# Performance work log

Measured on AMD Instinct MI355X. Metric: run time of the kernel, lower is better.

The kernel has to match this reference:

```python
import jax, jax.numpy as jnp
import numpy as np

B, S, D, H = 4, 2048, 1024, 16
HS = D // H  # head_size = 64


def setup_inputs() -> dict:
    key = jax.random.key(0)
    ks = jax.random.split(key, 6)
    scale = 0.02
    return {
        "token_embeddings": jax.random.normal(ks[0], (B, S, D), dtype=jnp.float32),
        # per-head projection weights, stacked: [H, D, HS] (x @ W per head)
        "Wq": jax.random.normal(ks[1], (H, D, HS), dtype=jnp.float32) * scale,
        "Wk": jax.random.normal(ks[2], (H, D, HS), dtype=jnp.float32) * scale,
        "Wv": jax.random.normal(ks[3], (H, D, HS), dtype=jnp.float32) * scale,
        # output projection (Linear with bias): y = x @ Wo + bo
        "Wo": jax.random.normal(ks[4], (D, D), dtype=jnp.float32) * scale,
        "bo": jax.random.normal(ks[5], (D,), dtype=jnp.float32) * scale,
    }


def reference(token_embeddings, Wq, Wk, Wv, Wo, bo):
    # Per-head projections, batched over heads: [B,H,S,HS]
    q = jnp.einsum("bsd,hde->bhse", token_embeddings, Wq)
    k = jnp.einsum("bsd,hde->bhse", token_embeddings, Wk)
    v = jnp.einsum("bsd,hde->bhse", token_embeddings, Wv)
    scale = HS ** -0.5
    scores = jnp.einsum("bhqe,bhke->bhqk", q, k) * scale  # [B,H,S,S]
    causal = jnp.tril(jnp.ones((S, S), dtype=bool))
    scores = jnp.where(causal, scores, -jnp.inf)
    weights = jax.nn.softmax(scores, axis=-1)
    # dropout in eval mode -> identity
    out = jnp.einsum("bhqk,bhke->bhqe", weights, v)  # [B,H,S,HS]
    # concat heads -> [B,S,D] (head order matches torch.cat over heads)
    out = out.transpose(0, 2, 1, 3).reshape(B, S, D)
    return out @ Wo + bo
```

## Files before the change

kernel.cpp:

```cpp
#include <hip/hip_runtime.h>


typedef __bf16 bf16;
typedef bf16 bf16x8 __attribute__((ext_vector_type(8)));
typedef bf16 bf16x4 __attribute__((ext_vector_type(4)));
typedef float f32x4 __attribute__((ext_vector_type(4)));

__device__ __forceinline__ void gload16(const void* gsrc, void* ldst) {
  __builtin_amdgcn_global_load_lds(
      (const __attribute__((address_space(1))) unsigned int*)gsrc,
      (__attribute__((address_space(3))) unsigned int*)ldst, 16, 0, 0);
}

__device__ __forceinline__ f32x4 mfma16(bf16x8 a, bf16x8 b, f32x4 c) {
  return __builtin_amdgcn_mfma_f32_16x16x32_bf16(a, b, c, 0, 0, 0);
}

__global__ __launch_bounds__(256) void pack_all_kernel(const float* __restrict__ x,
                                                       const float* __restrict__ Wq,
                                                       const float* __restrict__ Wk,
                                                       const float* __restrict__ Wv,
                                                       const float* __restrict__ Wo,
                                                       bf16* __restrict__ xb,
                                                       bf16* __restrict__ WT,
                                                       bf16* __restrict__ WoT) {
  const int stride = gridDim.x * 256;
  const int t0 = blockIdx.x * 256 + threadIdx.x;
  for (int i = t0; i < 2097152; i += stride) {
    float4 v = *(const float4*)(x + (size_t)i * 4);
    bf16x4 o;
    o[0] = (bf16)v.x; o[1] = (bf16)v.y; o[2] = (bf16)v.z; o[3] = (bf16)v.w;
    *(bf16x4*)(xb + (size_t)i * 4) = o;
  }
  for (int idx = t0; idx < 3145728; idx += stride) {
    int n = idx >> 10, k = idx & 1023;
    int sel = n >> 10, nn = n & 1023;
    const float* W = (sel == 0) ? Wq : (sel == 1 ? Wk : Wv);
    int h = nn >> 6, e = nn & 63;
    WT[(size_t)n * 1024 + k] = (bf16)W[h * 65536 + k * 64 + e];
  }
  for (int idx = t0; idx < 1048576; idx += stride) {
    int n = idx >> 10, k = idx & 1023;
    WoT[idx] = (bf16)Wo[k * 1024 + n];
  }
}

template <bool F32OUT>
__global__ __launch_bounds__(256, 2) void gemm4_kernel(const bf16* __restrict__ A,
                                                       const bf16* __restrict__ BT,
                                                       bf16* __restrict__ Cb,
                                                       float* __restrict__ Cf,
                                                       const float* __restrict__ bias,
                                                       int N, int K) {
  __shared__ bf16 As[2][128 * 64];
  __shared__ bf16 Bs[2][128 * 64];
  const int tid = threadIdx.x, lane = tid & 63, wave = tid >> 6;
  const int g = lane >> 4, c = lane & 15;
  const int wr = wave >> 1, wc = wave & 1;
  const int bid = blockIdx.x;
  const int xcd = bid & 7, local = bid >> 3;
  const int m0 = (xcd * 8 + (local & 7)) * 128;
  const int n0 = (local >> 3) * 128;

  const int schunk = (lane & 7) ^ (lane >> 3);

#define STAGE4(T, S)                                                      \
  do {                                                                    \
    _Pragma("unroll") for (int j = 0; j < 4; ++j) {                       \
      const int r = wave * 32 + j * 8 + (lane >> 3);                      \
      const int ldso = wave * 4096 + j * 1024 + lane * 16;                \
      gload16(A + (size_t)(m0 + r) * K + (T)*64 + schunk * 8,             \
              (char*)&As[S][0] + ldso);                                   \
      gload16(BT + (size_t)(n0 + r) * K + (T)*64 + schunk * 8,            \
              (char*)&Bs[S][0] + ldso);                                   \
    }                                                                     \
  } while (0)

  f32x4 acc[4][4] = {};
  const int nt = K >> 6;
  STAGE4(0, 0);
  asm volatile("s_waitcnt vmcnt(0)" ::: "memory");
  __builtin_amdgcn_sched_barrier(0);
  __builtin_amdgcn_s_barrier();
  __builtin_amdgcn_sched_barrier(0);

#pragma unroll 1
  for (int t = 0; t < nt; ++t) {
    const int s = t & 1;
    if (t + 1 < nt) STAGE4(t + 1, s ^ 1);
    bf16x8 af[4][2], bfr[4][2];
#pragma unroll
    for (int m = 0; m < 4; ++m) {
      const int row = wr * 64 + m * 16 + c;
#pragma unroll
      for (int kk = 0; kk < 2; ++kk)
        af[m][kk] = *(const bf16x8*)((const char*)&As[s][0] + row * 128 +
                                     (((kk * 4 + g) ^ (row & 7)) << 4));
    }
#pragma unroll
    for (int n = 0; n < 4; ++n) {
      const int row = wc * 64 + n * 16 + c;
#pragma unroll
      for (int kk = 0; kk < 2; ++kk)
        bfr[n][kk] = *(const bf16x8*)((const char*)&Bs[s][0] + row * 128 +
                                      (((kk * 4 + g) ^ (row & 7)) << 4));
    }
    __builtin_amdgcn_s_setprio(1);
#pragma unroll
    for (int kk = 0; kk < 2; ++kk)
#pragma unroll
      for (int m = 0; m < 4; ++m)
#pragma unroll
        for (int n = 0; n < 4; ++n)
          acc[m][n] = mfma16(af[m][kk], bfr[n][kk], acc[m][n]);
    __builtin_amdgcn_s_setprio(0);
    if (t + 1 < nt) {
      asm volatile("s_waitcnt vmcnt(0)" ::: "memory");
      __builtin_amdgcn_sched_barrier(0);
      __builtin_amdgcn_s_barrier();
      __builtin_amdgcn_sched_barrier(0);
    }
  }
#undef STAGE4
#pragma unroll
  for (int m = 0; m < 4; ++m)
#pragma unroll
    for (int n = 0; n < 4; ++n)
#pragma unroll
      for (int i = 0; i < 4; ++i) {
        int row = m0 + wr * 64 + m * 16 + g * 4 + i;
        int col = n0 + wc * 64 + n * 16 + c;
        if (F32OUT)
          Cf[(size_t)row * N + col] = acc[m][n][i] + bias[col];
        else
          Cb[(size_t)row * N + col] = (bf16)acc[m][n][i];
      }
}

__global__ __launch_bounds__(256) void transpose_v_kernel(const bf16* __restrict__ qkv,
                                                          bf16* __restrict__ vt) {
  __shared__ bf16 tl[64][72];
  const int tid = threadIdx.x;
  const int st = blockIdx.x, bh = blockIdx.y;
  const int b = bh >> 4, h = bh & 15;
#pragma unroll
  for (int it = 0; it < 2; ++it) {
    int idx = it * 256 + tid;
    int sl = idx >> 3, ch = idx & 7;
    bf16x8 v = *(const bf16x8*)(qkv + (size_t)(b * 2048 + st * 64 + sl) * 3072 + 2048 + h * 64 + ch * 8);
    *(bf16x8*)&tl[sl][ch * 8] = v;
  }
  __syncthreads();
#pragma unroll
  for (int it = 0; it < 2; ++it) {
    int idx = it * 256 + tid;
    int d = idx >> 3, ch = idx & 7;
    const int blk = ch >> 2, g = ch & 3;
    bf16x8 o;
#pragma unroll
    for (int j = 0; j < 8; ++j) {
      int loc = (j < 4) ? (4 * g + j) : (16 + 4 * g + (j - 4));
      o[j] = tl[blk * 32 + loc][d];
    }
    *(bf16x8*)(vt + ((size_t)bh * 64 + d) * 2048 + st * 64 + ch * 8) = o;
  }
}

__global__ __launch_bounds__(512, 4) void attn_kernel(const bf16* __restrict__ qkv,
                                                      const bf16* __restrict__ vt,
                                                      bf16* __restrict__ attn_out) {
  __shared__ bf16 Ks[2][128 * 64];
  __shared__ bf16 Vs[2][64 * 128];
  const int tid = threadIdx.x, lane = tid & 63, wave = tid >> 6;
  const int g = lane >> 4, c = lane & 15;
  const int bid = blockIdx.x;
  const int xcd = bid & 7;
  const int x = (bid >> 3) & 7;
  const int bh = (bid >> 6) * 8 + xcd;
  const int b = bh >> 4, h = bh & 15;
  const float SCL = 0.125f * 1.4426950408889634f;

  bf16x8 ones;
#pragma unroll
  for (int j = 0; j < 8; ++j) ones[j] = (bf16)1.0f;

#define STAGE(KT, BUF)                                                                    \
  do {                                                                                    \
    _Pragma("unroll") for (int t2 = 0; t2 < 2; ++t2) {                                    \
      int o = t2 * 8192 + wave * 1024 + lane * 16;                          \
      int rK = o >> 7, chK = (((o & 127) >> 4) ^ (rK & 7));                               \
      gload16((const char*)qkv +                                                          \
                  ((size_t)(b * 2048 + (KT)*128 + rK) * 3072 + 1024 + h * 64) * 2 +       \
                  (chK << 4),                                                             \
              (char*)Ks[BUF] + o);                                                        \
      int rV = o >> 8, chV = (((o & 255) >> 4) ^ (rV & 7));                               \
      gload16((const char*)vt + (((size_t)bh * 64 + rV) * 2048 + (KT)*128) * 2 +          \
                  (chV << 4),                                                             \
              (char*)Vs[BUF] + o);                                                        \
    }                                                                                     \
  } while (0)

#pragma unroll 1
  for (int ph = 0; ph < 2; ++ph) {
    const int qt = ph ? (15 - x) : x;
    const int qlow = qt * 128 + wave * 16;

    bf16x8 qf[2];
#pragma unroll
    for (int kk = 0; kk < 2; ++kk) {
      size_t row = (size_t)(b * 2048 + qlow + c);
      qf[kk] = *(const bf16x8*)(qkv + row * 3072 + h * 64 + kk * 32 + g * 8);
    }

    f32x4 oacc[4] = {};
    f32x4 lacc = {};
    float mrun = -3.0e38f;

    const int nkt = qt + 1;
    __builtin_amdgcn_s_barrier();
    __builtin_amdgcn_sched_barrier(0);
    STAGE(0, 0);
    asm volatile("s_waitcnt vmcnt(0)" ::: "memory");
    __builtin_amdgcn_sched_barrier(0);
    __builtin_amdgcn_s_barrier();
    __builtin_amdgcn_sched_barrier(0);
    for (int kt = 0; kt < nkt; ++kt) {
      const int cur = kt & 1;
      if (kt + 1 < nkt) STAGE(kt + 1, cur ^ 1);
      f32x4 sc[8] = {};
      __builtin_amdgcn_s_setprio(1);
#pragma unroll
      for (int n = 0; n < 8; ++n) {
        int key = n * 16 + c;
#pragma unroll
        for (int kk = 0; kk < 2; ++kk) {
          bf16x8 kf = *(const bf16x8*)((const char*)Ks[cur] + key * 128 +
                                       (((kk * 4 + g) ^ (key & 7)) << 4));
          sc[n] = mfma16(kf, qf[kk], sc[n]);
        }
      }
      __builtin_amdgcn_s_setprio(0);
      const int q = qlow + c;
      if (kt == qt) {
#pragma unroll
        for (int n = 0; n < 8; ++n)
#pragma unroll
          for (int i = 0; i < 4; ++i)
            sc[n][i] = ((kt * 128 + n * 16 + 4 * g + i) <= q) ? sc[n][i] : -3.0e38f;
      }
      float vmax;
      {
        float a[8];
#pragma unroll
        for (int n = 0; n < 8; ++n)
          a[n] = fmaxf(fmaxf(sc[n][0], sc[n][1]), fmaxf(sc[n][2], sc[n][3]));
        float b0 = fmaxf(a[0], a[1]), b1 = fmaxf(a[2], a[3]);
        float b2 = fmaxf(a[4], a[5]), b3 = fmaxf(a[6], a[7]);
        vmax = fmaxf(fmaxf(b0, b1), fmaxf(b2, b3));
      }
      vmax = fmaxf(vmax, __shfl_xor(vmax, 16));
      vmax = fmaxf(vmax, __shfl_xor(vmax, 32));
      const float mx = vmax * SCL;
      if (!__all(mx <= mrun + 8.0f)) {
        const float mnew = fmaxf(mrun, mx);
        const float fs = __builtin_amdgcn_exp2f(mrun - mnew);
        mrun = mnew;
#pragma unroll
        for (int i = 0; i < 4; ++i) {
          float fsb = __shfl(fs, ((lane >> 4) << 2) + i);
          lacc[i] *= fsb;
#pragma unroll
          for (int dn = 0; dn < 4; ++dn) oacc[dn][i] *= fsb;
        }
      }
#pragma unroll
      for (int n = 0; n < 8; ++n)
#pragma unroll
        for (int i = 0; i < 4; ++i)
          sc[n][i] = __builtin_amdgcn_exp2f(fmaf(sc[n][i], SCL, -mrun));
      bf16x8 pa[4];
#pragma unroll
      for (int kss = 0; kss < 4; ++kss) {
        bf16x8 t;
#pragma unroll
        for (int j = 0; j < 4; ++j) t[j] = (bf16)sc[2 * kss][j];
#pragma unroll
        for (int j = 0; j < 4; ++j) t[4 + j] = (bf16)sc[2 * kss + 1][j];
        pa[kss] = t;
      }
      __builtin_amdgcn_s_setprio(1);
#pragma unroll
      for (int kss = 0; kss < 4; ++kss) {
        lacc = mfma16(pa[kss], ones, lacc);
#pragma unroll
        for (int dn = 0; dn < 4; ++dn) {
          const int d = dn * 16 + c;
          bf16x8 vb = *(const bf16x8*)((const char*)Vs[cur] + d * 256 +
                                       (((kss * 4 + g) ^ (d & 7)) << 4));
          oacc[dn] = mfma16(pa[kss], vb, oacc[dn]);
        }
      }
      __builtin_amdgcn_s_setprio(0);
      if (kt + 1 < nkt) {
        asm volatile("s_waitcnt vmcnt(0)" ::: "memory");
        __builtin_amdgcn_sched_barrier(0);
        __builtin_amdgcn_s_barrier();
        __builtin_amdgcn_sched_barrier(0);
      }
    }
#pragma unroll
    for (int i = 0; i < 4; ++i) {
      float inv = __builtin_amdgcn_rcpf(lacc[i]);
      size_t row = (size_t)(b * 2048 + qlow + 4 * g + i);
#pragma unroll
      for (int dn = 0; dn < 4; ++dn)
        attn_out[row * 1024 + h * 64 + dn * 16 + c] = (bf16)(oacc[dn][i] * inv);
    }
  }
#undef STAGE
}

extern "C" void kernel_launch(void* const* d_in, const int* in_sizes, int n_in,
                              void* d_out, int out_size, void* d_ws, size_t ws_size,
                              hipStream_t stream) {
  const float* x  = (const float*)d_in[0];
  const float* Wq = (const float*)d_in[1];
  const float* Wk = (const float*)d_in[2];
  const float* Wv = (const float*)d_in[3];
  const float* Wo = (const float*)d_in[4];
  const float* bo = (const float*)d_in[5];
  float* out = (float*)d_out;
  char* ws = (char*)d_ws;

  bf16* Xb    = (bf16*)(ws);
  bf16* WqkvT = (bf16*)(ws + 16777216);
  bf16* WoT   = (bf16*)(ws + 23068672);
  bf16* QKV   = (bf16*)(ws + 25165824);
  bf16* VT    = (bf16*)(ws + 75497472);
  bf16* AttnO = (bf16*)(ws + 92274688);

  pack_all_kernel<<<2048, 256, 0, stream>>>(x, Wq, Wk, Wv, Wo, Xb, WqkvT, WoT);
  gemm4_kernel<false><<<1536, 256, 0, stream>>>(Xb, WqkvT, QKV, nullptr, nullptr,
                                                3072, 1024);
  transpose_v_kernel<<<dim3(32, 64), 256, 0, stream>>>(QKV, VT);
  attn_kernel<<<512, 512, 0, stream>>>(QKV, VT, AttnO);
  gemm4_kernel<true><<<512, 256, 0, stream>>>(AttnO, WoT, nullptr, out, bo,
                                              1024, 1024);
}
```

Baseline: 167.5 us.

## Give each attention wave two query sub-tiles to reuse K/V fragments

```diff
diff --git a/kernel.cpp b/kernel.cpp
--- a/kernel.cpp
+++ b/kernel.cpp
@@ -166,7 +166,7 @@
   }
 }
 
-__global__ __launch_bounds__(512, 4) void attn_kernel(const bf16* __restrict__ qkv,
+__global__ __launch_bounds__(256, 2) void attn_kernel(const bf16* __restrict__ qkv,
                                                       const bf16* __restrict__ vt,
                                                       bf16* __restrict__ attn_out) {
   __shared__ bf16 Ks[2][128 * 64];
@@ -186,8 +186,8 @@
 
 #define STAGE(KT, BUF)                                                                    \
   do {                                                                                    \
-    _Pragma("unroll") for (int t2 = 0; t2 < 2; ++t2) {                                    \
-      int o = t2 * 8192 + wave * 1024 + lane * 16;                          \
+    _Pragma("unroll") for (int t2 = 0; t2 < 4; ++t2) {                                    \
+      int o = t2 * 4096 + wave * 1024 + lane * 16;                          \
       int rK = o >> 7, chK = (((o & 127) >> 4) ^ (rK & 7));                               \
       gload16((const char*)qkv +                                                          \
                   ((size_t)(b * 2048 + (KT)*128 + rK) * 3072 + 1024 + h * 64) * 2 +       \
@@ -203,18 +203,20 @@
 #pragma unroll 1
   for (int ph = 0; ph < 2; ++ph) {
     const int qt = ph ? (15 - x) : x;
-    const int qlow = qt * 128 + wave * 16;
-
-    bf16x8 qf[2];
-#pragma unroll
-    for (int kk = 0; kk < 2; ++kk) {
-      size_t row = (size_t)(b * 2048 + qlow + c);
-      qf[kk] = *(const bf16x8*)(qkv + row * 3072 + h * 64 + kk * 32 + g * 8);
-    }
-
-    f32x4 oacc[4] = {};
-    f32x4 lacc = {};
-    float mrun = -3.0e38f;
+    const int qlow = qt * 128 + wave * 32;
+
+    bf16x8 qf[2][2];
+#pragma unroll
+    for (int m = 0; m < 2; ++m)
+#pragma unroll
+      for (int kk = 0; kk < 2; ++kk) {
+        size_t row = (size_t)(b * 2048 + qlow + m * 16 + c);
+        qf[m][kk] = *(const bf16x8*)(qkv + row * 3072 + h * 64 + kk * 32 + g * 8);
+      }
+
+    f32x4 oacc[2][4] = {};
+    f32x4 lacc[2] = {};
+    float mrun[2] = {-3.0e38f, -3.0e38f};
 
     const int nkt = qt + 1;
     __builtin_amdgcn_s_barrier();
@@ -227,7 +229,7 @@
     for (int kt = 0; kt < nkt; ++kt) {
       const int cur = kt & 1;
       if (kt + 1 < nkt) STAGE(kt + 1, cur ^ 1);
-      f32x4 sc[8] = {};
+      f32x4 sc[8][2] = {};
       __builtin_amdgcn_s_setprio(1);
 #pragma unroll
       for (int n = 0; n < 8; ++n) {
@@ -236,68 +238,79 @@
         for (int kk = 0; kk < 2; ++kk) {
           bf16x8 kf = *(const bf16x8*)((const char*)Ks[cur] + key * 128 +
                                        (((kk * 4 + g) ^ (key & 7)) << 4));
-          sc[n] = mfma16(kf, qf[kk], sc[n]);
+#pragma unroll
+          for (int m = 0; m < 2; ++m) sc[n][m] = mfma16(kf, qf[m][kk], sc[n][m]);
         }
       }
       __builtin_amdgcn_s_setprio(0);
-      const int q = qlow + c;
-      if (kt == qt) {
+      float mx[2];
+#pragma unroll
+      for (int m = 0; m < 2; ++m) {
+        const int q = qlow + m * 16 + c;
+        if (kt == qt) {
+#pragma unroll
+          for (int n = 0; n < 8; ++n)
+#pragma unroll
+            for (int i = 0; i < 4; ++i)
+              sc[n][m][i] = ((kt * 128 + n * 16 + 4 * g + i) <= q) ? sc[n][m][i] : -3.0e38f;
+        }
+        float a[8];
 #pragma unroll
         for (int n = 0; n < 8; ++n)
-#pragma unroll
-          for (int i = 0; i < 4; ++i)
-            sc[n][i] = ((kt * 128 + n * 16 + 4 * g + i) <= q) ? sc[n][i] : -3.0e38f;
-      }
-      float vmax;
-      {
-        float a[8];
-#pragma unroll
-        for (int n = 0; n < 8; ++n)
-          a[n] = fmaxf(fmaxf(sc[n][0], sc[n][1]), fmaxf(sc[n][2], sc[n][3]));
+          a[n] = fmaxf(fmaxf(sc[n][m][0], sc[n][m][1]), fmaxf(sc[n][m][2], sc[n][m][3]));
         float b0 = fmaxf(a[0], a[1]), b1 = fmaxf(a[2], a[3]);
         float b2 = fmaxf(a[4], a[5]), b3 = fmaxf(a[6], a[7]);
-        vmax = fmaxf(fmaxf(b0, b1), fmaxf(b2, b3));
-      }
-      vmax = fmaxf(vmax, __shfl_xor(vmax, 16));
-      vmax = fmaxf(vmax, __shfl_xor(vmax, 32));
-      const float mx = vmax * SCL;
-      if (!__all(mx <= mrun + 8.0f)) {
-        const float mnew = fmaxf(mrun, mx);
-        const float fs = __builtin_amdgcn_exp2f(mrun - mnew);
-        mrun = mnew;
-#pragma unroll
-        for (int i = 0; i < 4; ++i) {
-          float fsb = __shfl(fs, ((lane >> 4) << 2) + i);
-          lacc[i] *= fsb;
-#pragma unroll
-          for (int dn = 0; dn < 4; ++dn) oacc[dn][i] *= fsb;
-        }
-      }
-#pragma unroll
-      for (int n = 0; n < 8; ++n)
-#pragma unroll
-        for (int i = 0; i < 4; ++i)
-          sc[n][i] = __builtin_amdgcn_exp2f(fmaf(sc[n][i], SCL, -mrun));
-      bf16x8 pa[4];
+        float vmax = fmaxf(fmaxf(b0, b1), fmaxf(b2, b3));
+        vmax = fmaxf(vmax, __shfl_xor(vmax, 16));
+        vmax = fmaxf(vmax, __shfl_xor(vmax, 32));
+        mx[m] = vmax * SCL;
+      }
+      if (!__all(mx[0] <= mrun[0] + 8.0f && mx[1] <= mrun[1] + 8.0f)) {
+#pragma unroll
+        for (int m = 0; m < 2; ++m) {
+          const float mnew = fmaxf(mrun[m], mx[m]);
+          const float fs = __builtin_amdgcn_exp2f(mrun[m] - mnew);
+          mrun[m] = mnew;
+#pragma unroll
+          for (int i = 0; i < 4; ++i) {
+            float fsb = __shfl(fs, ((lane >> 4) << 2) + i);
+            lacc[m][i] *= fsb;
+#pragma unroll
+            for (int dn = 0; dn < 4; ++dn) oacc[m][dn][i] *= fsb;
+          }
+        }
+      }
+#pragma unroll
+      for (int m = 0; m < 2; ++m)
+#pragma unroll
+        for (int n = 0; n < 8; ++n)
+#pragma unroll
+          for (int i = 0; i < 4; ++i)
+            sc[n][m][i] = __builtin_amdgcn_exp2f(fmaf(sc[n][m][i], SCL, -mrun[m]));
+      bf16x8 pa[2][4];
+#pragma unroll
+      for (int m = 0; m < 2; ++m)
+#pragma unroll
+        for (int kss = 0; kss < 4; ++kss) {
+          bf16x8 t;
+#pragma unroll
+          for (int j = 0; j < 4; ++j) t[j] = (bf16)sc[2 * kss][m][j];
+#pragma unroll
+          for (int j = 0; j < 4; ++j) t[4 + j] = (bf16)sc[2 * kss + 1][m][j];
+          pa[m][kss] = t;
+        }
+      __builtin_amdgcn_s_setprio(1);
 #pragma unroll
       for (int kss = 0; kss < 4; ++kss) {
-        bf16x8 t;
-#pragma unroll
-        for (int j = 0; j < 4; ++j) t[j] = (bf16)sc[2 * kss][j];
-#pragma unroll
-        for (int j = 0; j < 4; ++j) t[4 + j] = (bf16)sc[2 * kss + 1][j];
-        pa[kss] = t;
-      }
-      __builtin_amdgcn_s_setprio(1);
-#pragma unroll
-      for (int kss = 0; kss < 4; ++kss) {
-        lacc = mfma16(pa[kss], ones, lacc);
+#pragma unroll
+        for (int m = 0; m < 2; ++m) lacc[m] = mfma16(pa[m][kss], ones, lacc[m]);
 #pragma unroll
         for (int dn = 0; dn < 4; ++dn) {
           const int d = dn * 16 + c;
           bf16x8 vb = *(const bf16x8*)((const char*)Vs[cur] + d * 256 +
                                        (((kss * 4 + g) ^ (d & 7)) << 4));
-          oacc[dn] = mfma16(pa[kss], vb, oacc[dn]);
+#pragma unroll
+          for (int m = 0; m < 2; ++m) oacc[m][dn] = mfma16(pa[m][kss], vb, oacc[m][dn]);
         }
       }
       __builtin_amdgcn_s_setprio(0);
@@ -309,13 +322,15 @@
       }
     }
 #pragma unroll
-    for (int i = 0; i < 4; ++i) {
-      float inv = __builtin_amdgcn_rcpf(lacc[i]);
-      size_t row = (size_t)(b * 2048 + qlow + 4 * g + i);
-#pragma unroll
-      for (int dn = 0; dn < 4; ++dn)
-        attn_out[row * 1024 + h * 64 + dn * 16 + c] = (bf16)(oacc[dn][i] * inv);
-    }
+    for (int m = 0; m < 2; ++m)
+#pragma unroll
+      for (int i = 0; i < 4; ++i) {
+        float inv = __builtin_amdgcn_rcpf(lacc[m][i]);
+        size_t row = (size_t)(b * 2048 + qlow + m * 16 + 4 * g + i);
+#pragma unroll
+        for (int dn = 0; dn < 4; ++dn)
+          attn_out[row * 1024 + h * 64 + dn * 16 + c] = (bf16)(oacc[m][dn][i] * inv);
+      }
   }
 #undef STAGE
 }
@@ -343,7 +358,7 @@
   gemm4_kernel<false><<<1536, 256, 0, stream>>>(Xb, WqkvT, QKV, nullptr, nullptr,
                                                 3072, 1024);
   transpose_v_kernel<<<dim3(32, 64), 256, 0, stream>>>(QKV, VT);
-  attn_kernel<<<512, 512, 0, stream>>>(QKV, VT, AttnO);
+  attn_kernel<<<512, 256, 0, stream>>>(QKV, VT, AttnO);
   gemm4_kernel<true><<<512, 256, 0, stream>>>(AttnO, WoT, nullptr, out, bo,
                                               1024, 1024);
 }
```

Measured after the change: 170.0 us. About the same (+1.5%).

## Use 256x256-tile 8-wave GEMM kernel for the QKV projection

Applied to the files above, without the earlier changes.

```diff
diff --git a/kernel.cpp b/kernel.cpp
--- a/kernel.cpp
+++ b/kernel.cpp
@@ -43,6 +43,95 @@
     int n = idx >> 10, k = idx & 1023;
     WoT[idx] = (bf16)Wo[k * 1024 + n];
   }
+}
+
+template <bool F32OUT>
+__global__ __launch_bounds__(512, 2) void gemm7_kernel(const bf16* __restrict__ A,
+                                                       const bf16* __restrict__ BT,
+                                                       bf16* __restrict__ Cb,
+                                                       float* __restrict__ Cf,
+                                                       const float* __restrict__ bias,
+                                                       int N, int K) {
+  __shared__ bf16 As[2][256 * 64];
+  __shared__ bf16 Bs[2][256 * 64];
+  const int tid = threadIdx.x, lane = tid & 63, wave = tid >> 6;
+  const int g = lane >> 4, c = lane & 15;
+  const int wr = wave >> 2, wc = wave & 3;
+  const int bid = blockIdx.x;
+  const int xcd = bid & 7, local = bid >> 3;
+  const int m0 = (xcd * 4 + (local & 3)) * 256;
+  const int n0 = (local >> 2) * 256;
+
+  const int sch = (tid & 7) ^ ((tid >> 3) & 7);
+
+#define STAGE7(T, S)                                                      \
+  do {                                                                    \
+    _Pragma("unroll") for (int j = 0; j < 4; ++j) {                       \
+      const int r = j * 64 + (tid >> 3);                                  \
+      const int ldso = j * 8192 + tid * 16;                               \
+      gload16(A + (size_t)(m0 + r) * K + (T)*64 + sch * 8,                \
+              (char*)&As[S][0] + ldso);                                   \
+      gload16(BT + (size_t)(n0 + r) * K + (T)*64 + sch * 8,               \
+              (char*)&Bs[S][0] + ldso);                                   \
+    }                                                                     \
+  } while (0)
+
+  f32x4 acc[8][4] = {};
+  const int nt = K >> 6;
+  STAGE7(0, 0);
+  asm volatile("s_waitcnt vmcnt(0)" ::: "memory");
+  __builtin_amdgcn_sched_barrier(0);
+  __builtin_amdgcn_s_barrier();
+  __builtin_amdgcn_sched_barrier(0);
+
+#pragma unroll 1
+  for (int t = 0; t < nt; ++t) {
+    const int s = t & 1;
+    if (t + 1 < nt) STAGE7(t + 1, s ^ 1);
+#pragma unroll
+    for (int kk = 0; kk < 2; ++kk) {
+      bf16x8 af[8], bfr[4];
+#pragma unroll
+      for (int m = 0; m < 8; ++m) {
+        const int row = wr * 128 + m * 16 + c;
+        af[m] = *(const bf16x8*)((const char*)&As[s][0] + row * 128 +
+                                 (((kk * 4 + g) ^ (row & 7)) << 4));
+      }
+#pragma unroll
+      for (int n = 0; n < 4; ++n) {
+        const int row = wc * 64 + n * 16 + c;
+        bfr[n] = *(const bf16x8*)((const char*)&Bs[s][0] + row * 128 +
+                                  (((kk * 4 + g) ^ (row & 7)) << 4));
+      }
+      __builtin_amdgcn_s_setprio(1);
+#pragma unroll
+      for (int m = 0; m < 8; ++m)
+#pragma unroll
+        for (int n = 0; n < 4; ++n)
+          acc[m][n] = mfma16(af[m], bfr[n], acc[m][n]);
+      __builtin_amdgcn_s_setprio(0);
+    }
+    if (t + 1 < nt) {
+      asm volatile("s_waitcnt vmcnt(0)" ::: "memory");
+      __builtin_amdgcn_sched_barrier(0);
+      __builtin_amdgcn_s_barrier();
+      __builtin_amdgcn_sched_barrier(0);
+    }
+  }
+#undef STAGE7
+#pragma unroll
+  for (int m = 0; m < 8; ++m)
+#pragma unroll
+    for (int n = 0; n < 4; ++n)
+#pragma unroll
+      for (int i = 0; i < 4; ++i) {
+        int row = m0 + wr * 128 + m * 16 + g * 4 + i;
+        int col = n0 + wc * 64 + n * 16 + c;
+        if (F32OUT)
+          Cf[(size_t)row * N + col] = acc[m][n][i] + bias[col];
+        else
+          Cb[(size_t)row * N + col] = (bf16)acc[m][n][i];
+      }
 }
 
 template <bool F32OUT>
@@ -340,8 +429,8 @@
   bf16* AttnO = (bf16*)(ws + 92274688);
 
   pack_all_kernel<<<2048, 256, 0, stream>>>(x, Wq, Wk, Wv, Wo, Xb, WqkvT, WoT);
-  gemm4_kernel<false><<<1536, 256, 0, stream>>>(Xb, WqkvT, QKV, nullptr, nullptr,
-                                                3072, 1024);
+  gemm7_kernel<false><<<384, 512, 0, stream>>>(Xb, WqkvT, QKV, nullptr, nullptr,
+                                               3072, 1024);
   transpose_v_kernel<<<dim3(32, 64), 256, 0, stream>>>(QKV, VT);
   attn_kernel<<<512, 512, 0, stream>>>(QKV, VT, AttnO);
   gemm4_kernel<true><<<512, 256, 0, stream>>>(AttnO, WoT, nullptr, out, bo,
```

After: 177.4 us. +5.9%, slower.
